# Kernel optimization log

Hardware: AMD Instinct MI355X
Metric: run time of the kernel (lower is better)

Reference implementation:

```python
import jax, jax.numpy as jnp
import numpy as np

N_NODES = 500_000
N_EDGES = 1_000_000
IN_DIM = 128
HID_DIM = 256
BN_EPS = 1e-5


def setup_inputs() -> dict:
    key = jax.random.key(0)
    ks = jax.random.split(key, 4)
    out = jax.random.normal(ks[0], (N_NODES, IN_DIM), dtype=jnp.float32)
    edge_label_index = jax.random.randint(ks[1], (2, N_EDGES), 0, N_NODES, dtype=jnp.int64)
    # Kaiming-uniform-ish init scale for linears
    W1 = jax.random.normal(ks[2], (IN_DIM, HID_DIM), dtype=jnp.float32) * (1.0 / np.sqrt(IN_DIM))
    b1 = jnp.zeros((HID_DIM,), dtype=jnp.float32)
    gamma = jnp.ones((HID_DIM,), dtype=jnp.float32)
    beta = jnp.zeros((HID_DIM,), dtype=jnp.float32)
    W2 = jax.random.normal(ks[3], (HID_DIM, 1), dtype=jnp.float32) * (1.0 / np.sqrt(HID_DIM))
    b2 = jnp.zeros((1,), dtype=jnp.float32)
    return {"out": out, "edge_label_index": edge_label_index,
            "W1": W1, "b1": b1, "gamma": gamma, "beta": beta, "W2": W2, "b2": b2}


def reference(out, edge_label_index, W1, b1, gamma, beta, W2, b2):
    src = edge_label_index[0]
    dst = edge_label_index[1]
    dot = out[src] * out[dst]                      # [E, IN_DIM] gather + hadamard
    h = dot @ W1 + b1                              # [E, HID_DIM]
    # BatchNorm1d (training mode: batch statistics, biased variance)
    mean = jnp.mean(h, axis=0)
    var = jnp.mean(jnp.square(h - mean), axis=0)
    h = (h - mean) * jax.lax.rsqrt(var + BN_EPS) * gamma + beta
    h = jax.nn.relu(h)
    y = h @ W2 + b2                                # [E, 1]
    return y.reshape(-1)
```

## Files before the change

### kernel.cpp

```cpp
#include <hip/hip_runtime.h>
#include <hip/hip_bf16.h>

#define E_EDGES   1000000
#define TILE_E    32
#define N_TILES   (E_EDGES / TILE_E)
#define IN_DIM_K  128
#define HID_N     256
#define BN_EPS_F  1e-5f
#define MAIN_GRID 512

typedef __attribute__((ext_vector_type(4))) float f32x4;
typedef __attribute__((ext_vector_type(8))) short bf16x8;

__device__ __forceinline__ unsigned short f2bf(float f) {
    __hip_bfloat16 h = __float2bfloat16(f);
    return *reinterpret_cast<unsigned short*>(&h);
}
__device__ __forceinline__ unsigned pack2(float lo, float hi) {
    return (unsigned)f2bf(lo) | ((unsigned)f2bf(hi) << 16);
}

union FragU { uint4 u; bf16x8 v; unsigned w[4]; };

__global__ void zero_stats_kernel(float* g) {
    g[threadIdx.x] = 0.0f;
}

__global__ void finalize_stats_kernel(const float* __restrict__ gstat,
                                      const float* __restrict__ gamma,
                                      const float* __restrict__ beta,
                                      float* __restrict__ nAB) {
    int c = threadIdx.x;
    float inv_e = 1.0f / (float)E_EDGES;
    float mean = gstat[c] * inv_e;
    float var  = fmaxf(gstat[256 + c] * inv_e - mean * mean, 0.0f);
    float a = gamma[c] * rsqrtf(var + BN_EPS_F);
    nAB[c] = a;
    nAB[256 + c] = beta[c] - mean * a;
}

template <bool STATS>
__global__ __launch_bounds__(256, 2)
void hadamard_mlp_kernel(const float* __restrict__ nodes,
                         const int* __restrict__ eidx,
                         const float* __restrict__ W1,
                         const float* __restrict__ W2,
                         const float* __restrict__ b2p,
                         float* __restrict__ gstat,
                         const float* __restrict__ nAB,
                         float* __restrict__ y)
{
    __shared__ unsigned sh_d[2][TILE_E * 68];
    __shared__ float s_red[2][128];

    const int tid  = threadIdx.x;
    const int lane = tid & 63;
    const int wn   = tid >> 6;
    const int l15  = lane & 15;
    const int l4   = lane >> 4;

    bf16x8 bfrag[4][4];
    #pragma unroll
    for (int nt = 0; nt < 4; ++nt) {
        const int c = wn * 64 + nt * 16 + l15;
        #pragma unroll
        for (int kk = 0; kk < 4; ++kk) {
            const int kb = kk * 32 + 8 * l4;
            FragU t;
            #pragma unroll
            for (int j = 0; j < 4; ++j) {
                float w0 = W1[(kb + 2 * j    ) * HID_N + c];
                float w1 = W1[(kb + 2 * j + 1) * HID_N + c];
                t.w[j] = pack2(w0, w1);
            }
            bfrag[nt][kk] = t.v;
        }
    }

    float a_n[4], b_n[4], w2_n[4];
    if (!STATS) {
        #pragma unroll
        for (int nt = 0; nt < 4; ++nt) {
            const int c = wn * 64 + nt * 16 + l15;
            a_n[nt]  = nAB[c];
            b_n[nt]  = nAB[256 + c];
            w2_n[nt] = W2[c];
        }
    }
    const float b2v = b2p[0];

    float s1[4] = {0.f, 0.f, 0.f, 0.f};
    float s2[4] = {0.f, 0.f, 0.f, 0.f};

    const int ge   = tid >> 3;
    const int part = tid & 7;

    float4 gA[8], gB[8];
    int siA, diA, siB, diB;

    const int t0 = blockIdx.x;
    {
        const int e0 = t0 * TILE_E + ge;
        const int s = eidx[e0];
        const int d = eidx[E_EDGES + e0];
        const float4* ps = reinterpret_cast<const float4*>(nodes + (size_t)s * IN_DIM_K) + part * 4;
        const float4* pd = reinterpret_cast<const float4*>(nodes + (size_t)d * IN_DIM_K) + part * 4;
        #pragma unroll
        for (int j = 0; j < 4; ++j) { gA[j] = ps[j]; gA[4 + j] = pd[j]; }
    }
    if (t0 + MAIN_GRID < N_TILES) {
        const int e1 = (t0 + MAIN_GRID) * TILE_E + ge;
        const int s = eidx[e1];
        const int d = eidx[E_EDGES + e1];
        const float4* ps = reinterpret_cast<const float4*>(nodes + (size_t)s * IN_DIM_K) + part * 4;
        const float4* pd = reinterpret_cast<const float4*>(nodes + (size_t)d * IN_DIM_K) + part * 4;
        #pragma unroll
        for (int j = 0; j < 4; ++j) { gB[j] = ps[j]; gB[4 + j] = pd[j]; }
    }
    siA = diA = siB = diB = 0;
    if (t0 + 2 * MAIN_GRID < N_TILES) {
        const int e = (t0 + 2 * MAIN_GRID) * TILE_E + ge;
        siA = eidx[e];  diA = eidx[E_EDGES + e];
    }
    if (t0 + 3 * MAIN_GRID < N_TILES) {
        const int e = (t0 + 3 * MAIN_GRID) * TILE_E + ge;
        siB = eidx[e];  diB = eidx[E_EDGES + e];
    }

    int cur = 0;
    int ptile = -1;

#define PIPE_BODY(TILE, GV, SIV, DIV)                                          \
    {                                                                          \
        const int tile_ = (TILE);                                              \
        {                       \
            unsigned buf[8];                                                   \
            _Pragma("unroll")                                                  \
            for (int j = 0; j < 4; ++j) {                                      \
                buf[2*j]   = pack2(GV[j].x * GV[4+j].x, GV[j].y * GV[4+j].y);  \
                buf[2*j+1] = pack2(GV[j].z * GV[4+j].z, GV[j].w * GV[4+j].w);  \
            }                                                                  \
            unsigned* dst = sh_d[cur] + ge * 68 + part * 8;                    \
            *reinterpret_cast<uint4*>(dst)     = *reinterpret_cast<const uint4*>(buf);     \
            *reinterpret_cast<uint4*>(dst + 4) = *reinterpret_cast<const uint4*>(buf + 4); \
        }                                                                      \
              \
        if (tile_ + 2 * MAIN_GRID < N_TILES) {                                 \
            const float4* ps = reinterpret_cast<const float4*>(nodes + (size_t)SIV * IN_DIM_K) + part * 4; \
            const float4* pd = reinterpret_cast<const float4*>(nodes + (size_t)DIV * IN_DIM_K) + part * 4; \
            _Pragma("unroll")                                                  \
            for (int j = 0; j < 4; ++j) { GV[j] = ps[j]; GV[4+j] = pd[j]; }    \
        }                                                                      \
                            \
        if (tile_ + 4 * MAIN_GRID < N_TILES) {                                 \
            const int e_ = (tile_ + 4 * MAIN_GRID) * TILE_E + ge;              \
            SIV = eidx[e_];  DIV = eidx[E_EDGES + e_];                         \
        }                                                                      \
        __syncthreads();                                                       \
                                     \
        if (!STATS && ptile >= 0 && tid < TILE_E) {                            \
            const float* r = s_red[cur ^ 1];                                   \
            y[ptile * TILE_E + tid] = r[tid] + r[32 + tid] + r[64 + tid]       \
                                    + r[96 + tid] + b2v;                       \
        }                                                                      \
                                  \
        f32x4 acc[2][4] = {};                                                  \
        __builtin_amdgcn_s_setprio(1);                                         \
        _Pragma("unroll")                                                      \
        for (int kk = 0; kk < 4; ++kk) {                                       \
            bf16x8 af[2];                                                      \
            _Pragma("unroll")                                                  \
            for (int mt = 0; mt < 2; ++mt) {                                   \
                const int row = mt * 16 + l15;                                 \
                FragU t;                                                       \
                t.u = *reinterpret_cast<const uint4*>(sh_d[cur] + row * 68 + kk * 16 + 4 * l4); \
                af[mt] = t.v;                                                  \
            }                                                                  \
            _Pragma("unroll")                                                  \
            for (int mt = 0; mt < 2; ++mt)                                     \
                _Pragma("unroll")                                              \
                for (int nt = 0; nt < 4; ++nt)                                 \
                    acc[mt][nt] = __builtin_amdgcn_mfma_f32_16x16x32_bf16(     \
                        af[mt], bfrag[nt][kk], acc[mt][nt], 0, 0, 0);          \
        }                                                                      \
        __builtin_amdgcn_s_setprio(0);                                         \
        if (STATS) {                                                           \
            _Pragma("unroll")                                                  \
            for (int nt = 0; nt < 4; ++nt) {                                   \
                float t1s = 0.f, t2s = 0.f;                                    \
                _Pragma("unroll")                                              \
                for (int mt = 0; mt < 2; ++mt)                                 \
                    _Pragma("unroll")                                          \
                    for (int r = 0; r < 4; ++r) {                              \
                        float v = acc[mt][nt][r];                              \
                        t1s += v;                                              \
                        t2s += v * v;                                          \
                    }                                                          \
                s1[nt] += t1s;                                                 \
                s2[nt] += t2s;                                                 \
            }                                                                  \
        } else {                                                               \
            float pw[2][4];                                                    \
            _Pragma("unroll")                                                  \
            for (int mt = 0; mt < 2; ++mt)                                     \
                _Pragma("unroll")                                              \
                for (int r = 0; r < 4; ++r) {                                  \
                    float acc_y = 0.f;                                         \
                    _Pragma("unroll")                                          \
                    for (int nt = 0; nt < 4; ++nt) {                           \
                        float z = acc[mt][nt][r] * a_n[nt] + b_n[nt];          \
                        z = fmaxf(z, 0.f);                                     \
                        acc_y += z * w2_n[nt];                                 \
                    }                                                          \
                    pw[mt][r] = acc_y;                                         \
                }                                                              \
            _Pragma("unroll")                                                  \
            for (int off = 1; off < 16; off <<= 1)                             \
                _Pragma("unroll")                                              \
                for (int mt = 0; mt < 2; ++mt)                                 \
                    _Pragma("unroll")                                          \
                    for (int r = 0; r < 4; ++r)                                \
                        pw[mt][r] += __shfl_xor(pw[mt][r], off, 64);           \
            if (l15 == 0) {                                                    \
                _Pragma("unroll")                                              \
                for (int mt = 0; mt < 2; ++mt)                                 \
                    _Pragma("unroll")                                          \
                    for (int r = 0; r < 4; ++r) {                              \
                        const int el = mt * 16 + l4 * 4 + r;                   \
                        s_red[cur][wn * 32 + el] = pw[mt][r];                  \
                    }                                                          \
            }                                                                  \
            ptile = tile_;                                                     \
        }                                                                      \
        cur ^= 1;                                                              \
    }

    for (int tile = t0; tile < N_TILES; tile += 2 * MAIN_GRID) {
        PIPE_BODY(tile, gA, siA, diA);
        const int tb = tile + MAIN_GRID;
        if (tb < N_TILES) {
            PIPE_BODY(tb, gB, siB, diB);
        }
    }
#undef PIPE_BODY

    if (STATS) {
        #pragma unroll
        for (int nt = 0; nt < 4; ++nt) {
            s1[nt] += __shfl_xor(s1[nt], 16, 64);
            s1[nt] += __shfl_xor(s1[nt], 32, 64);
            s2[nt] += __shfl_xor(s2[nt], 16, 64);
            s2[nt] += __shfl_xor(s2[nt], 32, 64);
        }
        if (l4 == 0) {
            #pragma unroll
            for (int nt = 0; nt < 4; ++nt) {
                const int c = wn * 64 + nt * 16 + l15;
                atomicAdd(&gstat[c],       s1[nt]);
                atomicAdd(&gstat[256 + c], s2[nt]);
            }
        }
    } else {
        __syncthreads();
        if (ptile >= 0 && tid < TILE_E) {
            const float* r = s_red[cur ^ 1];
            y[ptile * TILE_E + tid] = r[tid] + r[32 + tid] + r[64 + tid]
                                    + r[96 + tid] + b2v;
        }
    }
}

extern "C" void kernel_launch(void* const* d_in, const int* in_sizes, int n_in,
                              void* d_out, int out_size, void* d_ws, size_t ws_size,
                              hipStream_t stream) {
    const float* nodes = (const float*)d_in[0];
    const int*   eidx  = (const int*)d_in[1];
    const float* W1    = (const float*)d_in[2];
    const float* gamma = (const float*)d_in[4];
    const float* beta  = (const float*)d_in[5];
    const float* W2    = (const float*)d_in[6];
    const float* b2    = (const float*)d_in[7];

    float* ws    = (float*)d_ws;
    float* gstat = ws;
    float* nAB   = ws + 512;
    float* y     = (float*)d_out;

    zero_stats_kernel<<<1, 512, 0, stream>>>(gstat);
    hadamard_mlp_kernel<true><<<MAIN_GRID, 256, 0, stream>>>(
        nodes, eidx, W1, W2, b2, gstat, nAB, y);
    finalize_stats_kernel<<<1, 256, 0, stream>>>(gstat, gamma, beta, nAB);
    hadamard_mlp_kernel<false><<<MAIN_GRID, 256, 0, stream>>>(
        nodes, eidx, W1, W2, b2, gstat, nAB, y);
}
```

Before: 302.5 us.

## Cache bf16 hadamard products in workspace and stream them in pass two

The stats pass now also writes each edge's bf16 hadamard product row to a workspace buffer. A new streaming kernel then reads these rows contiguously for the normalize/ReLU/projection pass, instead of gathering both node rows again by random index. This trades a second random gather for a 256MB sequential write plus read. The path is taken only when the workspace is large enough, and otherwise falls back to the original two-gather scheme.

```diff
diff --git a/kernel.cpp b/kernel.cpp
--- a/kernel.cpp
+++ b/kernel.cpp
@@ -8,6 +8,7 @@
 #define HID_N     256
 #define BN_EPS_F  1e-5f
 #define MAIN_GRID 512
+#define P2_GRID   512
 
 typedef __attribute__((ext_vector_type(4))) float f32x4;
 typedef __attribute__((ext_vector_type(8))) short bf16x8;
@@ -39,7 +40,7 @@
     nAB[256 + c] = beta[c] - mean * a;
 }
 
-template <bool STATS>
+template <bool STATS, bool WRITE_D>
 __global__ __launch_bounds__(256, 2)
 void hadamard_mlp_kernel(const float* __restrict__ nodes,
                          const int* __restrict__ eidx,
@@ -48,6 +49,7 @@
                          const float* __restrict__ b2p,
                          float* __restrict__ gstat,
                          const float* __restrict__ nAB,
+                         unsigned* __restrict__ dbuf,
                          float* __restrict__ y)
 {
     __shared__ unsigned sh_d[2][TILE_E * 68];
@@ -133,7 +135,7 @@
 #define PIPE_BODY(TILE, GV, SIV, DIV)                                          \
     {                                                                          \
         const int tile_ = (TILE);                                              \
-        {                       \
+        {              \
             unsigned buf[8];                                                   \
             _Pragma("unroll")                                                  \
             for (int j = 0; j < 4; ++j) {                                      \
@@ -143,6 +145,11 @@
             unsigned* dst = sh_d[cur] + ge * 68 + part * 8;                    \
             *reinterpret_cast<uint4*>(dst)     = *reinterpret_cast<const uint4*>(buf);     \
             *reinterpret_cast<uint4*>(dst + 4) = *reinterpret_cast<const uint4*>(buf + 4); \
+            if (WRITE_D) {                                                     \
+                unsigned* dw = dbuf + (size_t)(tile_ * TILE_E + ge) * 64 + part * 8;       \
+                *reinterpret_cast<uint4*>(dw)     = *reinterpret_cast<const uint4*>(buf);     \
+                *reinterpret_cast<uint4*>(dw + 4) = *reinterpret_cast<const uint4*>(buf + 4); \
+            }                                                                  \
         }                                                                      \
               \
         if (tile_ + 2 * MAIN_GRID < N_TILES) {                                 \
@@ -270,6 +277,146 @@
     }
 }
 
+__global__ __launch_bounds__(256, 2)
+void pass2_stream_kernel(const unsigned* __restrict__ dbuf,
+                         const float* __restrict__ W1,
+                         const float* __restrict__ W2,
+                         const float* __restrict__ b2p,
+                         const float* __restrict__ nAB,
+                         float* __restrict__ y)
+{
+    __shared__ float s_red[2][128];
+
+    const int tid  = threadIdx.x;
+    const int lane = tid & 63;
+    const int wn   = tid >> 6;
+    const int l15  = lane & 15;
+    const int l4   = lane >> 4;
+
+    bf16x8 bfrag[4][4];
+    #pragma unroll
+    for (int nt = 0; nt < 4; ++nt) {
+        const int c = wn * 64 + nt * 16 + l15;
+        #pragma unroll
+        for (int kk = 0; kk < 4; ++kk) {
+            const int kb = kk * 32 + 8 * l4;
+            FragU t;
+            #pragma unroll
+            for (int j = 0; j < 4; ++j) {
+                float w0 = W1[(kb + 2 * j    ) * HID_N + c];
+                float w1 = W1[(kb + 2 * j + 1) * HID_N + c];
+                t.w[j] = pack2(w0, w1);
+            }
+            bfrag[nt][kk] = t.v;
+        }
+    }
+
+    float a_n[4], b_n[4], w2_n[4];
+    #pragma unroll
+    for (int nt = 0; nt < 4; ++nt) {
+        const int c = wn * 64 + nt * 16 + l15;
+        a_n[nt]  = nAB[c];
+        b_n[nt]  = nAB[256 + c];
+        w2_n[nt] = W2[c];
+    }
+    const float b2v = b2p[0];
+
+    const unsigned lbase = (unsigned)l15 * 64 + (unsigned)l4 * 4;
+
+    uint4 fA[8], fB[8];
+#define LOADF(F, TILE_)                                                        \
+    {   const unsigned* p = dbuf + (size_t)(TILE_) * 2048 + lbase;             \
+        _Pragma("unroll")                                                      \
+        for (int mt = 0; mt < 2; ++mt)                                         \
+            _Pragma("unroll")                                                  \
+            for (int kk = 0; kk < 4; ++kk)                                     \
+                F[mt * 4 + kk] = *reinterpret_cast<const uint4*>(p + mt * 1024 + kk * 16); \
+    }
+
+    const int t0 = blockIdx.x;
+    LOADF(fA, t0);
+
+    int cur = 0;
+    int ptile = -1;
+
+#define P2_BODY(TILE, FC, FN)                                                  \
+    {                                                                          \
+        const int tile_ = (TILE);                                              \
+        const int ntile_ = tile_ + P2_GRID;                                    \
+        if (ntile_ < N_TILES) LOADF(FN, ntile_);                               \
+        __syncthreads();                                                       \
+        if (ptile >= 0 && tid < TILE_E) {                                      \
+            const float* r = s_red[cur ^ 1];                                   \
+            y[ptile * TILE_E + tid] = r[tid] + r[32 + tid] + r[64 + tid]       \
+                                    + r[96 + tid] + b2v;                       \
+        }                                                                      \
+        f32x4 acc[2][4] = {};                                                  \
+        __builtin_amdgcn_s_setprio(1);                                         \
+        _Pragma("unroll")                                                      \
+        for (int kk = 0; kk < 4; ++kk) {                                       \
+            _Pragma("unroll")                                                  \
+            for (int mt = 0; mt < 2; ++mt) {                                   \
+                FragU t;                                                       \
+                t.u = FC[mt * 4 + kk];                                         \
+                _Pragma("unroll")                                              \
+                for (int nt = 0; nt < 4; ++nt)                                 \
+                    acc[mt][nt] = __builtin_amdgcn_mfma_f32_16x16x32_bf16(     \
+                        t.v, bfrag[nt][kk], acc[mt][nt], 0, 0, 0);             \
+            }                                                                  \
+        }                                                                      \
+        __builtin_amdgcn_s_setprio(0);                                         \
+        float pw[2][4];                                                        \
+        _Pragma("unroll")                                                      \
+        for (int mt = 0; mt < 2; ++mt)                                         \
+            _Pragma("unroll")                                                  \
+            for (int r = 0; r < 4; ++r) {                                      \
+                float acc_y = 0.f;                                             \
+                _Pragma("unroll")                                              \
+                for (int nt = 0; nt < 4; ++nt) {                               \
+                    float z = acc[mt][nt][r] * a_n[nt] + b_n[nt];              \
+                    z = fmaxf(z, 0.f);                                         \
+                    acc_y += z * w2_n[nt];                                     \
+                }                                                              \
+                pw[mt][r] = acc_y;                                             \
+            }                                                                  \
+        _Pragma("unroll")                                                      \
+        for (int off = 1; off < 16; off <<= 1)                                 \
+            _Pragma("unroll")                                                  \
+            for (int mt = 0; mt < 2; ++mt)                                     \
+                _Pragma("unroll")                                              \
+                for (int r = 0; r < 4; ++r)                                    \
+                    pw[mt][r] += __shfl_xor(pw[mt][r], off, 64);               \
+        if (l15 == 0) {                                                        \
+            _Pragma("unroll")                                                  \
+            for (int mt = 0; mt < 2; ++mt)                                     \
+                _Pragma("unroll")                                              \
+                for (int r = 0; r < 4; ++r) {                                  \
+                    const int el = mt * 16 + l4 * 4 + r;                       \
+                    s_red[cur][wn * 32 + el] = pw[mt][r];                      \
+                }                                                              \
+        }                                                                      \
+        ptile = tile_;                                                         \
+        cur ^= 1;                                                              \
+    }
+
+    for (int tile = t0; tile < N_TILES; tile += 2 * P2_GRID) {
+        P2_BODY(tile, fA, fB);
+        const int tb = tile + P2_GRID;
+        if (tb < N_TILES) {
+            P2_BODY(tb, fB, fA);
+        }
+    }
+#undef P2_BODY
+#undef LOADF
+
+    __syncthreads();
+    if (ptile >= 0 && tid < TILE_E) {
+        const float* r = s_red[cur ^ 1];
+        y[ptile * TILE_E + tid] = r[tid] + r[32 + tid] + r[64 + tid]
+                                + r[96 + tid] + b2v;
+    }
+}
+
 extern "C" void kernel_launch(void* const* d_in, const int* in_sizes, int n_in,
                               void* d_out, int out_size, void* d_ws, size_t ws_size,
                               hipStream_t stream) {
@@ -284,12 +431,24 @@
     float* ws    = (float*)d_ws;
     float* gstat = ws;
     float* nAB   = ws + 512;
+    unsigned* dbuf = (unsigned*)((char*)d_ws + 4096);
     float* y     = (float*)d_out;
 
+    const size_t D_BYTES = (size_t)E_EDGES * IN_DIM_K * 2;
+    const bool fast = ws_size >= (4096 + D_BYTES);
+
     zero_stats_kernel<<<1, 512, 0, stream>>>(gstat);
-    hadamard_mlp_kernel<true><<<MAIN_GRID, 256, 0, stream>>>(
-        nodes, eidx, W1, W2, b2, gstat, nAB, y);
-    finalize_stats_kernel<<<1, 256, 0, stream>>>(gstat, gamma, beta, nAB);
-    hadamard_mlp_kernel<false><<<MAIN_GRID, 256, 0, stream>>>(
-        nodes, eidx, W1, W2, b2, gstat, nAB, y);
-}
+    if (fast) {
+        hadamard_mlp_kernel<true, true><<<MAIN_GRID, 256, 0, stream>>>(
+            nodes, eidx, W1, W2, b2, gstat, nAB, dbuf, y);
+        finalize_stats_kernel<<<1, 256, 0, stream>>>(gstat, gamma, beta, nAB);
+        pass2_stream_kernel<<<P2_GRID, 256, 0, stream>>>(
+            dbuf, W1, W2, b2, nAB, y);
+    } else {
+        hadamard_mlp_kernel<true, false><<<MAIN_GRID, 256, 0, stream>>>(
+            nodes, eidx, W1, W2, b2, gstat, nAB, dbuf, y);
+        finalize_stats_kernel<<<1, 256, 0, stream>>>(gstat, gamma, beta, nAB);
+        hadamard_mlp_kernel<false, false><<<MAIN_GRID, 256, 0, stream>>>(
+            nodes, eidx, W1, W2, b2, gstat, nAB, dbuf, y);
+    }
+}
```

Measured after the change: 334.2 us. +10.5%, slower.

## Pre-convert node features to bf16 table and gather half-width rows

Applied to the files above, without the earlier changes.

Adds a conversion kernel that writes node features into a bf16 copy in the workspace, then both MLP passes gather 256-byte bf16 rows instead of 512-byte fp32 rows and multiply in unpacked bf16. This halves gather traffic per pass at the cost of one extra streaming conversion pass, and rounds inputs to bf16 before the hadamard product. The main grid also doubles to 1024 blocks. A fallback keeps the fp32 path when the workspace is too small.

```diff
diff --git a/kernel.cpp b/kernel.cpp
--- a/kernel.cpp
+++ b/kernel.cpp
@@ -1,13 +1,15 @@
 #include <hip/hip_runtime.h>
 #include <hip/hip_bf16.h>
 
+#define N_NODES   500000
 #define E_EDGES   1000000
 #define TILE_E    32
 #define N_TILES   (E_EDGES / TILE_E)
 #define IN_DIM_K  128
 #define HID_N     256
 #define BN_EPS_F  1e-5f
-#define MAIN_GRID 512
+#define MAIN_GRID 1024
+#define CONV_GRID 2048
 
 typedef __attribute__((ext_vector_type(4))) float f32x4;
 typedef __attribute__((ext_vector_type(8))) short bf16x8;
@@ -19,11 +21,35 @@
 __device__ __forceinline__ unsigned pack2(float lo, float hi) {
     return (unsigned)f2bf(lo) | ((unsigned)f2bf(hi) << 16);
 }
+__device__ __forceinline__ unsigned bfmul2(unsigned a, unsigned b) {
+    float alo = __uint_as_float(a << 16);
+    float ahi = __uint_as_float(a & 0xffff0000u);
+    float blo = __uint_as_float(b << 16);
+    float bhi = __uint_as_float(b & 0xffff0000u);
+    return pack2(alo * blo, ahi * bhi);
+}
 
 union FragU { uint4 u; bf16x8 v; unsigned w[4]; };
 
 __global__ void zero_stats_kernel(float* g) {
     g[threadIdx.x] = 0.0f;
+}
+
+__global__ void convert_nodes_kernel(const float* __restrict__ in,
+                                     unsigned* __restrict__ out) {
+    const size_t n4 = (size_t)N_NODES * IN_DIM_K / 8;
+    size_t i = (size_t)blockIdx.x * blockDim.x + threadIdx.x;
+    const size_t stride = (size_t)gridDim.x * blockDim.x;
+    for (; i < n4; i += stride) {
+        float4 a = reinterpret_cast<const float4*>(in)[2 * i];
+        float4 b = reinterpret_cast<const float4*>(in)[2 * i + 1];
+        uint4 o;
+        o.x = pack2(a.x, a.y);
+        o.y = pack2(a.z, a.w);
+        o.z = pack2(b.x, b.y);
+        o.w = pack2(b.z, b.w);
+        reinterpret_cast<uint4*>(out)[i] = o;
+    }
 }
 
 __global__ void finalize_stats_kernel(const float* __restrict__ gstat,
@@ -39,9 +65,10 @@
     nAB[256 + c] = beta[c] - mean * a;
 }
 
-template <bool STATS>
+template <bool STATS, bool BFT>
 __global__ __launch_bounds__(256, 2)
 void hadamard_mlp_kernel(const float* __restrict__ nodes,
+                         const unsigned* __restrict__ nbf,
                          const int* __restrict__ eidx,
                          const float* __restrict__ W1,
                          const float* __restrict__ W2,
@@ -95,27 +122,48 @@
     const int ge   = tid >> 3;
     const int part = tid & 7;
 
-    float4 gA[8], gB[8];
+    uint4  gA[4], gB[4];
+    float4 hA[8], hB[8];
     int siA, diA, siB, diB;
+
+#define GATHER(GV, HV, SNODE, DNODE)                                           \
+    if constexpr (BFT) {                                                       \
+        const uint4* ps = reinterpret_cast<const uint4*>(nbf + (size_t)(SNODE) * 64) + part * 2; \
+        const uint4* pd = reinterpret_cast<const uint4*>(nbf + (size_t)(DNODE) * 64) + part * 2; \
+        GV[0] = ps[0]; GV[1] = ps[1]; GV[2] = pd[0]; GV[3] = pd[1];            \
+    } else {                                                                   \
+        const float4* ps = reinterpret_cast<const float4*>(nodes + (size_t)(SNODE) * IN_DIM_K) + part * 4; \
+        const float4* pd = reinterpret_cast<const float4*>(nodes + (size_t)(DNODE) * IN_DIM_K) + part * 4; \
+        _Pragma("unroll")                                                      \
+        for (int j = 0; j < 4; ++j) { HV[j] = ps[j]; HV[4 + j] = pd[j]; }      \
+    }
+
+#define PACKBUF(GV, HV, buf)                                                   \
+    if constexpr (BFT) {                                                       \
+        buf[0] = bfmul2(GV[0].x, GV[2].x); buf[1] = bfmul2(GV[0].y, GV[2].y);  \
+        buf[2] = bfmul2(GV[0].z, GV[2].z); buf[3] = bfmul2(GV[0].w, GV[2].w);  \
+        buf[4] = bfmul2(GV[1].x, GV[3].x); buf[5] = bfmul2(GV[1].y, GV[3].y);  \
+        buf[6] = bfmul2(GV[1].z, GV[3].z); buf[7] = bfmul2(GV[1].w, GV[3].w);  \
+    } else {                                                                   \
+        _Pragma("unroll")                                                      \
+        for (int j = 0; j < 4; ++j) {                                          \
+            buf[2*j]   = pack2(HV[j].x * HV[4+j].x, HV[j].y * HV[4+j].y);      \
+            buf[2*j+1] = pack2(HV[j].z * HV[4+j].z, HV[j].w * HV[4+j].w);      \
+        }                                                                      \
+    }
 
     const int t0 = blockIdx.x;
     {
         const int e0 = t0 * TILE_E + ge;
         const int s = eidx[e0];
         const int d = eidx[E_EDGES + e0];
-        const float4* ps = reinterpret_cast<const float4*>(nodes + (size_t)s * IN_DIM_K) + part * 4;
-        const float4* pd = reinterpret_cast<const float4*>(nodes + (size_t)d * IN_DIM_K) + part * 4;
-        #pragma unroll
-        for (int j = 0; j < 4; ++j) { gA[j] = ps[j]; gA[4 + j] = pd[j]; }
+        GATHER(gA, hA, s, d);
     }
     if (t0 + MAIN_GRID < N_TILES) {
         const int e1 = (t0 + MAIN_GRID) * TILE_E + ge;
         const int s = eidx[e1];
         const int d = eidx[E_EDGES + e1];
-        const float4* ps = reinterpret_cast<const float4*>(nodes + (size_t)s * IN_DIM_K) + part * 4;
-        const float4* pd = reinterpret_cast<const float4*>(nodes + (size_t)d * IN_DIM_K) + part * 4;
-        #pragma unroll
-        for (int j = 0; j < 4; ++j) { gB[j] = ps[j]; gB[4 + j] = pd[j]; }
+        GATHER(gB, hB, s, d);
     }
     siA = diA = siB = diB = 0;
     if (t0 + 2 * MAIN_GRID < N_TILES) {
@@ -130,26 +178,19 @@
     int cur = 0;
     int ptile = -1;
 
-#define PIPE_BODY(TILE, GV, SIV, DIV)                                          \
+#define PIPE_BODY(TILE, GV, HV, SIV, DIV)                                      \
     {                                                                          \
         const int tile_ = (TILE);                                              \
         {                       \
             unsigned buf[8];                                                   \
-            _Pragma("unroll")                                                  \
-            for (int j = 0; j < 4; ++j) {                                      \
-                buf[2*j]   = pack2(GV[j].x * GV[4+j].x, GV[j].y * GV[4+j].y);  \
-                buf[2*j+1] = pack2(GV[j].z * GV[4+j].z, GV[j].w * GV[4+j].w);  \
-            }                                                                  \
+            PACKBUF(GV, HV, buf);                                              \
             unsigned* dst = sh_d[cur] + ge * 68 + part * 8;                    \
             *reinterpret_cast<uint4*>(dst)     = *reinterpret_cast<const uint4*>(buf);     \
             *reinterpret_cast<uint4*>(dst + 4) = *reinterpret_cast<const uint4*>(buf + 4); \
         }                                                                      \
               \
         if (tile_ + 2 * MAIN_GRID < N_TILES) {                                 \
-            const float4* ps = reinterpret_cast<const float4*>(nodes + (size_t)SIV * IN_DIM_K) + part * 4; \
-            const float4* pd = reinterpret_cast<const float4*>(nodes + (size_t)DIV * IN_DIM_K) + part * 4; \
-            _Pragma("unroll")                                                  \
-            for (int j = 0; j < 4; ++j) { GV[j] = ps[j]; GV[4+j] = pd[j]; }    \
+            GATHER(GV, HV, SIV, DIV);                                          \
         }                                                                      \
                             \
         if (tile_ + 4 * MAIN_GRID < N_TILES) {                                 \
@@ -236,13 +277,15 @@
     }
 
     for (int tile = t0; tile < N_TILES; tile += 2 * MAIN_GRID) {
-        PIPE_BODY(tile, gA, siA, diA);
+        PIPE_BODY(tile, gA, hA, siA, diA);
         const int tb = tile + MAIN_GRID;
         if (tb < N_TILES) {
-            PIPE_BODY(tb, gB, siB, diB);
+            PIPE_BODY(tb, gB, hB, siB, diB);
         }
     }
 #undef PIPE_BODY
+#undef GATHER
+#undef PACKBUF
 
     if (STATS) {
         #pragma unroll
@@ -284,12 +327,25 @@
     float* ws    = (float*)d_ws;
     float* gstat = ws;
     float* nAB   = ws + 512;
+    unsigned* nbf = (unsigned*)((char*)d_ws + 4096);
     float* y     = (float*)d_out;
 
+    const size_t T_BYTES = (size_t)N_NODES * IN_DIM_K * 2;
+    const bool fast = ws_size >= (4096 + T_BYTES);
+
     zero_stats_kernel<<<1, 512, 0, stream>>>(gstat);
-    hadamard_mlp_kernel<true><<<MAIN_GRID, 256, 0, stream>>>(
-        nodes, eidx, W1, W2, b2, gstat, nAB, y);
-    finalize_stats_kernel<<<1, 256, 0, stream>>>(gstat, gamma, beta, nAB);
-    hadamard_mlp_kernel<false><<<MAIN_GRID, 256, 0, stream>>>(
-        nodes, eidx, W1, W2, b2, gstat, nAB, y);
-}
+    if (fast) {
+        convert_nodes_kernel<<<CONV_GRID, 256, 0, stream>>>(nodes, nbf);
+        hadamard_mlp_kernel<true, true><<<MAIN_GRID, 256, 0, stream>>>(
+            nodes, nbf, eidx, W1, W2, b2, gstat, nAB, y);
+        finalize_stats_kernel<<<1, 256, 0, stream>>>(gstat, gamma, beta, nAB);
+        hadamard_mlp_kernel<false, true><<<MAIN_GRID, 256, 0, stream>>>(
+            nodes, nbf, eidx, W1, W2, b2, gstat, nAB, y);
+    } else {
+        hadamard_mlp_kernel<true, false><<<MAIN_GRID, 256, 0, stream>>>(
+            nodes, nbf, eidx, W1, W2, b2, gstat, nAB, y);
+        finalize_stats_kernel<<<1, 256, 0, stream>>>(gstat, gamma, beta, nAB);
+        hadamard_mlp_kernel<false, false><<<MAIN_GRID, 256, 0, stream>>>(
+            nodes, nbf, eidx, W1, W2, b2, gstat, nAB, y);
+    }
+}
```

Result: faster. 270.5 us (-10.6%).
